# Kernel optimization log

Hardware: AMD Instinct MI355X
Metric: run time of the kernel (lower is better)

Reference implementation:

```python
import jax, jax.numpy as jnp
import numpy as np

N_EMBD = 768
HIDDEN = 4 * N_EMBD
N_EXPERTS = 8
TOP_K = 2


def setup_inputs() -> dict:
    key = jax.random.key(0)
    ks = jax.random.split(key, 4)
    B, T, C, E, H = 4, 2048, N_EMBD, N_EXPERTS, HIDDEN
    x = jax.random.normal(ks[0], (B, T, C), dtype=jnp.float32)
    gate_w = jax.random.normal(ks[1], (E, C), dtype=jnp.float32) * 0.02
    gate_b = jnp.zeros((E,), dtype=jnp.float32)
    w_fc = jax.random.normal(ks[2], (E, H, C), dtype=jnp.float32) * 0.02
    b_fc = jnp.zeros((E, H), dtype=jnp.float32)
    w_proj = jax.random.normal(ks[3], (E, C, H), dtype=jnp.float32) * 0.02
    b_proj = jnp.zeros((E, C), dtype=jnp.float32)
    return {"x": x, "gate_w": gate_w, "gate_b": gate_b, "w_fc": w_fc,
            "b_fc": b_fc, "w_proj": w_proj, "b_proj": b_proj}


def reference(x, gate_w, gate_b, w_fc, b_fc, w_proj, b_proj):
    B, T, C = x.shape
    E = gate_b.shape[0]
    xf = x.reshape(-1, C)  # [N, C]
    # gating: Linear(C -> E), top-k, softmax over the k selected scores
    scores = xf @ gate_w.T + gate_b                      # [N, E]
    top_s, top_i = jax.lax.top_k(scores, TOP_K)          # [N, K]
    gates = jax.nn.softmax(top_s, axis=-1)               # [N, K]
    # combine weight per (token, expert): sum_k gate[t,k] * 1[top_i[t,k]==e]
    comb = jnp.sum(jax.nn.one_hot(top_i, E, dtype=xf.dtype) * gates[..., None], axis=1)  # [N, E]
    out = jnp.zeros_like(xf)
    for j in range(E):  # loop over fixed small expert count
        h = jax.nn.gelu(xf @ w_fc[j].T + b_fc[j], approximate=True)  # [N, H]
        y = h @ w_proj[j].T + b_proj[j]                              # [N, C]
        out = out + comb[:, j:j + 1] * y
    return out.reshape(B, T, C)
```

## Files before the change

### kernel.cpp

```cpp
#include <hip/hip_runtime.h>
#include <cmath>

#define N_TOK 8192
#define C_DIM 768
#define H_DIM 3072
#define NEXP  8
#define PADCAP 17408
#define MAXMT  136

typedef short short8 __attribute__((ext_vector_type(8)));
typedef float f32x4  __attribute__((ext_vector_type(4)));

__device__ __forceinline__ unsigned short f2b(float f) {
  unsigned int u = __float_as_uint(f);
  u += 0x7fffu + ((u >> 16) & 1u);
  return (unsigned short)(u >> 16);
}
__device__ __forceinline__ float b2f(unsigned short u) {
  return __uint_as_float((unsigned int)u << 16);
}
__device__ __forceinline__ void gll(const char* g, char* l) {
  __builtin_amdgcn_global_load_lds((const __attribute__((address_space(1))) void*)g,
                                   (__attribute__((address_space(3))) void*)l, 16, 0, 0);
}

__global__ __launch_bounds__(256) void gate_kernel(
    const float* __restrict__ x, const float* __restrict__ gw,
    const float* __restrict__ gb, int* __restrict__ counts,
    int* __restrict__ tok_e, int* __restrict__ tok_r, float* __restrict__ tok_w) {
  __shared__ float gwl[NEXP * C_DIM];
  __shared__ double red[256][NEXP];
  int tid = threadIdx.x;
  const float4* gw4 = (const float4*)gw;
  float4* gl4 = (float4*)gwl;
  for (int i = tid; i < NEXP * C_DIM / 4; i += 256) gl4[i] = gw4[i];
  __syncthreads();
  int tl = tid & 63;
  int kc = tid >> 6;
  int t = blockIdx.x * 64 + tl;
  double acc[NEXP];
#pragma unroll
  for (int e = 0; e < NEXP; e++) acc[e] = 0.0;
  const float* xr = x + (size_t)t * C_DIM;
  for (int k = kc * 192; k < kc * 192 + 192; k++) {
    double xv = (double)xr[k];
#pragma unroll
    for (int e = 0; e < NEXP; e++) acc[e] += xv * (double)gwl[e * C_DIM + k];
  }
#pragma unroll
  for (int e = 0; e < NEXP; e++) red[tid][e] = acc[e];
  __syncthreads();
  if (tid < 64) {
    double s[NEXP];
#pragma unroll
    for (int e = 0; e < NEXP; e++)
      s[e] = (double)gb[e] + red[tid][e] + red[tid + 64][e] + red[tid + 128][e] + red[tid + 192][e];
    double best = s[0], sec = -1e300; int bi = 0, si = -1;
#pragma unroll
    for (int e = 1; e < NEXP; e++) {
      if (s[e] > best)      { sec = best; si = bi; best = s[e]; bi = e; }
      else if (s[e] > sec)  { sec = s[e]; si = e; }
    }
    double ex = exp(sec - best);
    double den = 1.0 + ex;
    tok_e[2 * t] = bi;  tok_e[2 * t + 1] = si;
    tok_w[2 * t] = (float)(1.0 / den);  tok_w[2 * t + 1] = (float)(ex / den);
    tok_r[2 * t]     = atomicAdd(&counts[bi], 1);
    tok_r[2 * t + 1] = atomicAdd(&counts[si], 1);
  }
}

__global__ void offsets_kernel(const int* __restrict__ counts, int* __restrict__ po) {
  if (threadIdx.x == 0 && blockIdx.x == 0) {
    int s = 0;
    for (int e = 0; e < NEXP; e++) { po[e] = s; s += (counts[e] + 127) & ~127; }
    po[NEXP] = s;
  }
}

__global__ __launch_bounds__(256) void scatter_kernel(
    const int* __restrict__ tok_e, const int* __restrict__ tok_r,
    const float* __restrict__ tok_w, const int* __restrict__ po,
    int* __restrict__ perm_t, float* __restrict__ perm_w,
    int* __restrict__ tok_pos) {
  int t = blockIdx.x * 256 + threadIdx.x;
#pragma unroll
  for (int k = 0; k < 2; k++) {
    int e = tok_e[2 * t + k];
    int pos = po[e] + tok_r[2 * t + k];
    perm_t[pos] = t;
    perm_w[pos] = tok_w[2 * t + k];
    tok_pos[2 * t + k] = pos;
  }
}

__global__ __launch_bounds__(256) void gather_kernel(
    const float* __restrict__ x, const int* __restrict__ po,
    const int* __restrict__ perm_t, unsigned short* __restrict__ xg) {
  int row = blockIdx.x * 4 + (threadIdx.x >> 6);
  if (row >= po[NEXP]) return;
  int l = threadIdx.x & 63;
  int t = perm_t[row];
  const float4* src = (const float4*)(x + (size_t)t * C_DIM);
  ushort4* dst = (ushort4*)(xg + (size_t)row * C_DIM);
#pragma unroll
  for (int j = 0; j < 3; j++) {
    float4 v = src[l + j * 64];
    ushort4 o; o.x = f2b(v.x); o.y = f2b(v.y); o.z = f2b(v.z); o.w = f2b(v.w);
    dst[l + j * 64] = o;
  }
}

__global__ __launch_bounds__(256) void wconv_kernel(
    const float* __restrict__ wfc, const float* __restrict__ wproj,
    unsigned short* __restrict__ wfcb, unsigned short* __restrict__ wpjb) {
  const int n4 = NEXP * H_DIM * C_DIM / 4;
  int stride = gridDim.x * blockDim.x;
  for (int i = blockIdx.x * blockDim.x + threadIdx.x; i < 2 * n4; i += stride) {
    const float4* s; ushort4* d; int j;
    if (i < n4) { s = (const float4*)wfc;   d = (ushort4*)wfcb; j = i; }
    else        { s = (const float4*)wproj; d = (ushort4*)wpjb; j = i - n4; }
    float4 v = s[j];
    ushort4 o; o.x = f2b(v.x); o.y = f2b(v.y); o.z = f2b(v.z); o.w = f2b(v.w);
    d[j] = o;
  }
}

#define STAGE6(kt, bufbase) do {                                   \
    size_t kb_ = (size_t)(kt) * 128;                               \
    char* nb_ = lds + (bufbase);                                   \
    gll(gA0 + kb_, nb_ + wb);                                      \
    gll(gA1 + kb_, nb_ + 8192 + wb);                               \
    gll(gB0p + kb_, nb_ + 16384 + wb);                             \
    gll(gB1p + kb_, nb_ + 24576 + wb);                             \
    gll(gB2p + kb_, nb_ + 32768 + wb);                             \
    gll(gB3p + kb_, nb_ + 40960 + wb);                             \
  } while (0)

__device__ __forceinline__ void gemm_big(
    const unsigned short* A, int lda, const unsigned short* B, int ldb, int K,
    char* lds, int tid, f32x4 acc[4][4]) {
  const int w = tid >> 6, l = tid & 63;
  const int wr = w >> 2, wc = w & 3;
  const int ra0 = wr * 64 + (l & 15);
  const int rb0 = wc * 64 + (l & 15);
  const int kc = l >> 4;
  const int sa0 = (kc ^ ((ra0 >> 1) & 7)) * 16;
  const int sb0 = (kc ^ ((rb0 >> 1) & 7)) * 16;
  const int rA0 = tid >> 3,           cA0 = (tid & 7) ^ ((rA0 >> 1) & 7);
  const int rA1 = (512 + tid) >> 3,   cA1 = ((512 + tid) & 7) ^ ((rA1 >> 1) & 7);
  const int rB0 = tid >> 3,           cB0 = (tid & 7) ^ ((rB0 >> 1) & 7);
  const int rB1 = (512 + tid) >> 3,   cB1 = ((512 + tid) & 7) ^ ((rB1 >> 1) & 7);
  const int rB2 = (1024 + tid) >> 3,  cB2 = ((1024 + tid) & 7) ^ ((rB2 >> 1) & 7);
  const int rB3 = (1536 + tid) >> 3,  cB3 = ((1536 + tid) & 7) ^ ((rB3 >> 1) & 7);
  const char* gA0  = (const char*)(A + (size_t)rA0 * lda) + cA0 * 16;
  const char* gA1  = (const char*)(A + (size_t)rA1 * lda) + cA1 * 16;
  const char* gB0p = (const char*)(B + (size_t)rB0 * ldb) + cB0 * 16;
  const char* gB1p = (const char*)(B + (size_t)rB1 * ldb) + cB1 * 16;
  const char* gB2p = (const char*)(B + (size_t)rB2 * ldb) + cB2 * 16;
  const char* gB3p = (const char*)(B + (size_t)rB3 * ldb) + cB3 * 16;
  const int wb = w * 1024;
  const int iters = K >> 6;
  STAGE6(0, 0);
  STAGE6(1, 49152);
  int bc = 0, bn2 = 98304;
#pragma unroll 1
  for (int kt = 0; kt < iters; kt++) {
    if (kt < iters - 1) asm volatile("s_waitcnt vmcnt(6)\n\ts_barrier" ::: "memory");
    else                asm volatile("s_waitcnt vmcnt(0)\n\ts_barrier" ::: "memory");
    if (kt + 2 < iters) STAGE6(kt + 2, bn2);
    char* bb = lds + bc;
#pragma unroll
    for (int s = 0; s < 2; s++) {
      const int sxa = sa0 ^ (s << 6);
      const int sxb = sb0 ^ (s << 6);
      short8 af[4], bf[4];
#pragma unroll
      for (int mi = 0; mi < 4; mi++)
        af[mi] = *(const short8*)(bb + (ra0 + mi * 16) * 128 + sxa);
#pragma unroll
      for (int ni = 0; ni < 4; ni++)
        bf[ni] = *(const short8*)(bb + 16384 + (rb0 + ni * 16) * 128 + sxb);
      __builtin_amdgcn_s_setprio(1);
#pragma unroll
      for (int mi = 0; mi < 4; mi++)
#pragma unroll
        for (int ni = 0; ni < 4; ni++)
          acc[mi][ni] = __builtin_amdgcn_mfma_f32_16x16x32_bf16(af[mi], bf[ni], acc[mi][ni], 0, 0, 0);
      __builtin_amdgcn_s_setprio(0);
      if (s == 0) asm volatile("s_barrier" ::: "memory");
    }
    bc += 49152;  if (bc == 147456)  bc = 0;
    bn2 += 49152; if (bn2 == 147456) bn2 = 0;
  }
}

__global__ __launch_bounds__(512, 2) void fc1_kernel(
    const unsigned short* __restrict__ xg, const unsigned short* __restrict__ wfcb,
    const float* __restrict__ bfc, const int* __restrict__ po,
    unsigned short* __restrict__ h) {
  __shared__ char lds[147456];
  int bid = blockIdx.x;
  int r8 = bid & 7, g8 = bid >> 3;
  int col = g8 % 12;
  int Sp  = g8 / 12;
  int y   = r8 * 17 + Sp;
  int row0 = y * 128;
  if (row0 >= po[NEXP]) return;
  int e = 0;
#pragma unroll
  for (int i = 1; i < NEXP; i++) if (row0 >= po[i]) e = i;
  int n0 = col * 256;
  int tid = threadIdx.x;
  f32x4 acc[4][4];
#pragma unroll
  for (int mi = 0; mi < 4; mi++)
#pragma unroll
    for (int ni = 0; ni < 4; ni++) acc[mi][ni] = (f32x4){0.f, 0.f, 0.f, 0.f};
  gemm_big(xg + (size_t)row0 * C_DIM, C_DIM,
           wfcb + (size_t)e * H_DIM * C_DIM + (size_t)n0 * C_DIM, C_DIM, C_DIM,
           lds, tid, acc);
  int w = tid >> 6, l = tid & 63;
  int wr = w >> 2, wc = w & 3, q = l >> 4;
  const float* bias = bfc + (size_t)e * H_DIM;
#pragma unroll
  for (int ni = 0; ni < 4; ni++) {
    int colw = n0 + wc * 64 + ni * 16 + (l & 15);
    float bv = bias[colw];
#pragma unroll
    for (int mi = 0; mi < 4; mi++) {
#pragma unroll
      for (int r = 0; r < 4; r++) {
        int row = row0 + wr * 64 + mi * 16 + q * 4 + r;
        float v = acc[mi][ni][r] + bv;
        float z = v * fmaf(0.0356774081f, v * v, 0.7978845608f);
        float ex = __builtin_amdgcn_exp2f(-2.8853900818f * z);
        float g = v * __builtin_amdgcn_rcpf(1.0f + ex);
        h[(size_t)row * H_DIM + colw] = f2b(g);
      }
    }
  }
}

__global__ __launch_bounds__(512, 2) void fc2_kernel(
    const unsigned short* __restrict__ h, const unsigned short* __restrict__ wpjb,
    const float* __restrict__ bproj, const int* __restrict__ po,
    const float* __restrict__ perm_w, unsigned short* __restrict__ part) {
  __shared__ char lds[147456];
  int bid = blockIdx.x;
  int r8 = bid & 7, g8 = bid >> 3;
  int col = g8 % 3;
  int qq  = g8 / 3;
  int z   = qq & 1;
  int Sp  = qq >> 1;
  int y   = r8 * 17 + Sp;
  int row0 = y * 128;
  if (row0 >= po[NEXP]) return;
  int e = 0;
#pragma unroll
  for (int i = 1; i < NEXP; i++) if (row0 >= po[i]) e = i;
  int n0 = col * 256;
  int koff = z * (H_DIM / 2);
  int tid = threadIdx.x;
  f32x4 acc[4][4];
#pragma unroll
  for (int mi = 0; mi < 4; mi++)
#pragma unroll
    for (int ni = 0; ni < 4; ni++) acc[mi][ni] = (f32x4){0.f, 0.f, 0.f, 0.f};
  gemm_big(h + (size_t)row0 * H_DIM + koff, H_DIM,
           wpjb + (size_t)e * C_DIM * H_DIM + (size_t)n0 * H_DIM + koff, H_DIM, H_DIM / 2,
           lds, tid, acc);
  int w = tid >> 6, l = tid & 63;
  int wr = w >> 2, wc = w & 3, q = l >> 4;
  const float* bias = bproj + (size_t)e * C_DIM;
  unsigned short* pz = part + (size_t)z * PADCAP * C_DIM;
#pragma unroll
  for (int mi = 0; mi < 4; mi++) {
#pragma unroll
    for (int r = 0; r < 4; r++) {
      int pos = row0 + wr * 64 + mi * 16 + q * 4 + r;
      float wgt = perm_w[pos];
#pragma unroll
      for (int ni = 0; ni < 4; ni++) {
        int colw = n0 + wc * 64 + ni * 16 + (l & 15);
        float v = acc[mi][ni][r];
        if (z == 0) v += bias[colw];
        pz[(size_t)pos * C_DIM + colw] = f2b(v * wgt);
      }
    }
  }
}

__global__ __launch_bounds__(256) void combine_kernel(
    const unsigned short* __restrict__ part, const int* __restrict__ tok_pos,
    float* __restrict__ out) {
  const int NC4 = C_DIM / 4;
  int idx = blockIdx.x * 256 + threadIdx.x;
  int t = idx / NC4, c4 = idx - t * NC4;
  int p0 = tok_pos[2 * t], p1 = tok_pos[2 * t + 1];
  const size_t SP = (size_t)PADCAP * C_DIM;
  const unsigned short* r00 = part + (size_t)p0 * C_DIM + c4 * 4;
  const unsigned short* r10 = part + (size_t)p1 * C_DIM + c4 * 4;
  ushort4 v00 = *(const ushort4*)r00;
  ushort4 v01 = *(const ushort4*)(r00 + SP);
  ushort4 v10 = *(const ushort4*)r10;
  ushort4 v11 = *(const ushort4*)(r10 + SP);
  float4 o;
  o.x = b2f(v00.x) + b2f(v01.x) + b2f(v10.x) + b2f(v11.x);
  o.y = b2f(v00.y) + b2f(v01.y) + b2f(v10.y) + b2f(v11.y);
  o.z = b2f(v00.z) + b2f(v01.z) + b2f(v10.z) + b2f(v11.z);
  o.w = b2f(v00.w) + b2f(v01.w) + b2f(v10.w) + b2f(v11.w);
  ((float4*)out)[idx] = o;
}

extern "C" void kernel_launch(void* const* d_in, const int* in_sizes, int n_in,
                              void* d_out, int out_size, void* d_ws, size_t ws_size,
                              hipStream_t stream) {
  const float* x     = (const float*)d_in[0];
  const float* gw    = (const float*)d_in[1];
  const float* gb    = (const float*)d_in[2];
  const float* wfc   = (const float*)d_in[3];
  const float* bfc   = (const float*)d_in[4];
  const float* wproj = (const float*)d_in[5];
  const float* bproj = (const float*)d_in[6];
  float* out = (float*)d_out;
  char* ws = (char*)d_ws;

  int*   counts  = (int*)(ws + 0);
  int*   po      = (int*)(ws + 64);
  int*   tok_e   = (int*)(ws + 256);
  int*   tok_r   = (int*)(ws + 65792);
  float* tok_w   = (float*)(ws + 131328);
  int*   tok_pos = (int*)(ws + 196864);
  int*   perm_t  = (int*)(ws + 262400);
  float* perm_w  = (float*)(ws + 332032);
  const size_t ROUT_END = 401920;
  unsigned short* wpjb = (unsigned short*)(ws + 401920);
  unsigned short* hbuf = (unsigned short*)(ws + 38150656);
  unsigned short* xg   = (unsigned short*)(ws + 145105408);
  unsigned short* wfcb = (unsigned short*)(ws + 171844096);
  unsigned short* part = (unsigned short*)(ws + 145105408);

  hipMemsetAsync(ws, 0, ROUT_END, stream);

  gate_kernel<<<N_TOK / 64, 256, 0, stream>>>(x, gw, gb, counts, tok_e, tok_r, tok_w);
  offsets_kernel<<<1, 64, 0, stream>>>(counts, po);
  scatter_kernel<<<N_TOK / 256, 256, 0, stream>>>(tok_e, tok_r, tok_w, po, perm_t, perm_w, tok_pos);
  gather_kernel<<<PADCAP / 4, 256, 0, stream>>>(x, po, perm_t, xg);
  wconv_kernel<<<2048, 256, 0, stream>>>(wfc, wproj, wfcb, wpjb);
  fc1_kernel<<<8 * 17 * 12, 512, 0, stream>>>(xg, wfcb, bfc, po, hbuf);
  fc2_kernel<<<8 * 17 * 3 * 2, 512, 0, stream>>>(hbuf, wpjb, bproj, po, perm_w, part);
  combine_kernel<<<N_TOK * (C_DIM / 4) / 256, 256, 0, stream>>>(part, tok_pos, out);
}
```

Baseline: 533.7 us.

## Switch expert GEMMs to 256x256 tiles with ping-pong LDS schedule

Replaces the 128x256 triple-buffered GEMM core with a 256x256 tile per block, using two 64KB LDS buffers and interleaved quarter-tile MFMA phases that overlap global_load_lds with compute. Expert row padding grows to 256, fc2 drops its K-split so combine reads two partials instead of four, and the weight conversion is split so fc_proj conversion reuses the same workspace after fc1. Larger tiles raise operand reuse and remove the split-K traffic, at the cost of more padding waste, fewer blocks, higher register pressure and less parallelism in fc2.

```diff
diff --git a/kernel.cpp b/kernel.cpp
--- a/kernel.cpp
+++ b/kernel.cpp
@@ -5,8 +5,7 @@
 #define C_DIM 768
 #define H_DIM 3072
 #define NEXP  8
-#define PADCAP 17408
-#define MAXMT  136
+#define PADCAP 18432
 
 typedef short short8 __attribute__((ext_vector_type(8)));
 typedef float f32x4  __attribute__((ext_vector_type(4)));
@@ -73,7 +72,7 @@
 __global__ void offsets_kernel(const int* __restrict__ counts, int* __restrict__ po) {
   if (threadIdx.x == 0 && blockIdx.x == 0) {
     int s = 0;
-    for (int e = 0; e < NEXP; e++) { po[e] = s; s += (counts[e] + 127) & ~127; }
+    for (int e = 0; e < NEXP; e++) { po[e] = s; s += (counts[e] + 255) & ~255; }
     po[NEXP] = s;
   }
 }
@@ -112,126 +111,146 @@
 }
 
 __global__ __launch_bounds__(256) void wconv_kernel(
-    const float* __restrict__ wfc, const float* __restrict__ wproj,
-    unsigned short* __restrict__ wfcb, unsigned short* __restrict__ wpjb) {
-  const int n4 = NEXP * H_DIM * C_DIM / 4;
+    const float* __restrict__ src, unsigned short* __restrict__ dst, int n4) {
   int stride = gridDim.x * blockDim.x;
-  for (int i = blockIdx.x * blockDim.x + threadIdx.x; i < 2 * n4; i += stride) {
-    const float4* s; ushort4* d; int j;
-    if (i < n4) { s = (const float4*)wfc;   d = (ushort4*)wfcb; j = i; }
-    else        { s = (const float4*)wproj; d = (ushort4*)wpjb; j = i - n4; }
-    float4 v = s[j];
+  for (int i = blockIdx.x * blockDim.x + threadIdx.x; i < n4; i += stride) {
+    float4 v = ((const float4*)src)[i];
     ushort4 o; o.x = f2b(v.x); o.y = f2b(v.y); o.z = f2b(v.z); o.w = f2b(v.w);
-    d[j] = o;
-  }
-}
-
-#define STAGE6(kt, bufbase) do {                                   \
-    size_t kb_ = (size_t)(kt) * 128;                               \
-    char* nb_ = lds + (bufbase);                                   \
-    gll(gA0 + kb_, nb_ + wb);                                      \
-    gll(gA1 + kb_, nb_ + 8192 + wb);                               \
-    gll(gB0p + kb_, nb_ + 16384 + wb);                             \
-    gll(gB1p + kb_, nb_ + 24576 + wb);                             \
-    gll(gB2p + kb_, nb_ + 32768 + wb);                             \
-    gll(gB3p + kb_, nb_ + 40960 + wb);                             \
-  } while (0)
-
-__device__ __forceinline__ void gemm_big(
-    const unsigned short* A, int lda, const unsigned short* B, int ldb, int K,
-    char* lds, int tid, f32x4 acc[4][4]) {
+    ((ushort4*)dst)[i] = o;
+  }
+}
+
+__device__ __forceinline__ void gemm8p(
+    const char* __restrict__ Ab, size_t ldaB,
+    const char* __restrict__ Bb, size_t ldbB, int ktiles,
+    char* lds, int tid, f32x4 acc[8][4]) {
   const int w = tid >> 6, l = tid & 63;
   const int wr = w >> 2, wc = w & 3;
-  const int ra0 = wr * 64 + (l & 15);
-  const int rb0 = wc * 64 + (l & 15);
-  const int kc = l >> 4;
-  const int sa0 = (kc ^ ((ra0 >> 1) & 7)) * 16;
-  const int sb0 = (kc ^ ((rb0 >> 1) & 7)) * 16;
-  const int rA0 = tid >> 3,           cA0 = (tid & 7) ^ ((rA0 >> 1) & 7);
-  const int rA1 = (512 + tid) >> 3,   cA1 = ((512 + tid) & 7) ^ ((rA1 >> 1) & 7);
-  const int rB0 = tid >> 3,           cB0 = (tid & 7) ^ ((rB0 >> 1) & 7);
-  const int rB1 = (512 + tid) >> 3,   cB1 = ((512 + tid) & 7) ^ ((rB1 >> 1) & 7);
-  const int rB2 = (1024 + tid) >> 3,  cB2 = ((1024 + tid) & 7) ^ ((rB2 >> 1) & 7);
-  const int rB3 = (1536 + tid) >> 3,  cB3 = ((1536 + tid) & 7) ^ ((rB3 >> 1) & 7);
-  const char* gA0  = (const char*)(A + (size_t)rA0 * lda) + cA0 * 16;
-  const char* gA1  = (const char*)(A + (size_t)rA1 * lda) + cA1 * 16;
-  const char* gB0p = (const char*)(B + (size_t)rB0 * ldb) + cB0 * 16;
-  const char* gB1p = (const char*)(B + (size_t)rB1 * ldb) + cB1 * 16;
-  const char* gB2p = (const char*)(B + (size_t)rB2 * ldb) + cB2 * 16;
-  const char* gB3p = (const char*)(B + (size_t)rB3 * ldb) + cB3 * 16;
-  const int wb = w * 1024;
-  const int iters = K >> 6;
-  STAGE6(0, 0);
-  STAGE6(1, 49152);
-  int bc = 0, bn2 = 98304;
+  const int lr = l & 15, kc = l >> 4;
+  const int sw = (lr >> 1) & 7;
+  const int s0 = ((kc ^ sw) << 4);
+  const int s1 = s0 ^ 64;
+  const int arow = ((wr << 7) + lr) << 7;
+  const int brow = 32768 + (((wc << 6) + lr) << 7);
+  const int rl0 = tid >> 3;
+  const int cg0 = (tid & 7) ^ ((rl0 >> 1) & 7);
+  const size_t oA0 = (size_t)rl0 * ldaB + (cg0 << 4);
+  const size_t oA1 = oA0 + (ldaB << 6);
+  const size_t oB0 = (size_t)rl0 * ldbB + (cg0 << 4);
+  const size_t oB1 = oB0 + (ldbB << 6);
+  const int wb = w << 10;
+
+#define SA(b, h, kt) do { \
+    const char* s_ = Ab + (size_t)(h) * 128 * ldaB + (size_t)(kt) * 128; \
+    gll(s_ + oA0, lds + (b) * 65536 + (h) * 16384 + wb); \
+    gll(s_ + oA1, lds + (b) * 65536 + (h) * 16384 + 8192 + wb); } while (0)
+#define SB(b, h, kt) do { \
+    const char* s_ = Bb + (size_t)(h) * 128 * ldbB + (size_t)(kt) * 128; \
+    gll(s_ + oB0, lds + (b) * 65536 + 32768 + (h) * 16384 + wb); \
+    gll(s_ + oB1, lds + (b) * 65536 + 32768 + (h) * 16384 + 8192 + wb); } while (0)
+#define BAR() asm volatile("s_barrier" ::: "memory")
+#define RDA(B, mb) do { \
+    for (int mi = 0; mi < 4; mi++) { \
+      af[mi][0] = *(const short8*)(lds + (B) + arow + ((mb) + mi) * 2048 + s0); \
+      af[mi][1] = *(const short8*)(lds + (B) + arow + ((mb) + mi) * 2048 + s1); } } while (0)
+#define RDB(B, nb) do { \
+    for (int ni = 0; ni < 2; ni++) { \
+      bf[(nb) + ni][0] = *(const short8*)(lds + (B) + brow + ((nb) + ni) * 2048 + s0); \
+      bf[(nb) + ni][1] = *(const short8*)(lds + (B) + brow + ((nb) + ni) * 2048 + s1); } } while (0)
+#define MM(mb, nb) do { \
+    __builtin_amdgcn_s_setprio(1); \
+    for (int mi = 0; mi < 4; mi++) \
+      for (int ni = 0; ni < 2; ni++) \
+        for (int kk = 0; kk < 2; kk++) \
+          acc[(mb) + mi][(nb) + ni] = __builtin_amdgcn_mfma_f32_16x16x32_bf16( \
+              af[mi][kk], bf[(nb) + ni][kk], acc[(mb) + mi][(nb) + ni], 0, 0, 0); \
+    __builtin_amdgcn_s_setprio(0); } while (0)
+
+  short8 af[4][2], bf[4][2];
+  SB(0, 0, 0); SB(0, 1, 0); SA(0, 0, 0); SA(0, 1, 0);
+  SB(1, 0, 1); SB(1, 1, 1);
+  asm volatile("s_waitcnt vmcnt(4)" ::: "memory");
+  BAR();
+  const int iters = ktiles >> 1;
 #pragma unroll 1
-  for (int kt = 0; kt < iters; kt++) {
-    if (kt < iters - 1) asm volatile("s_waitcnt vmcnt(6)\n\ts_barrier" ::: "memory");
-    else                asm volatile("s_waitcnt vmcnt(0)\n\ts_barrier" ::: "memory");
-    if (kt + 2 < iters) STAGE6(kt + 2, bn2);
-    char* bb = lds + bc;
-#pragma unroll
-    for (int s = 0; s < 2; s++) {
-      const int sxa = sa0 ^ (s << 6);
-      const int sxb = sb0 ^ (s << 6);
-      short8 af[4], bf[4];
-#pragma unroll
-      for (int mi = 0; mi < 4; mi++)
-        af[mi] = *(const short8*)(bb + (ra0 + mi * 16) * 128 + sxa);
-#pragma unroll
-      for (int ni = 0; ni < 4; ni++)
-        bf[ni] = *(const short8*)(bb + 16384 + (rb0 + ni * 16) * 128 + sxb);
-      __builtin_amdgcn_s_setprio(1);
-#pragma unroll
-      for (int mi = 0; mi < 4; mi++)
-#pragma unroll
-        for (int ni = 0; ni < 4; ni++)
-          acc[mi][ni] = __builtin_amdgcn_mfma_f32_16x16x32_bf16(af[mi], bf[ni], acc[mi][ni], 0, 0, 0);
-      __builtin_amdgcn_s_setprio(0);
-      if (s == 0) asm volatile("s_barrier" ::: "memory");
+  for (int i = 0; i < iters; i++) {
+    const int t1 = 2 * i + 1, t2 = 2 * i + 2, t3 = 2 * i + 3;
+    const bool nl = (i + 1 < iters);
+    RDA(0, 0); RDB(0, 0);
+    SA(1, 0, t1);
+    BAR(); MM(0, 0); BAR();
+    RDB(0, 2);
+    SA(1, 1, t1);
+    BAR(); MM(0, 2); BAR();
+    RDA(0, 4);
+    if (nl) SB(0, 0, t2);
+    BAR(); MM(4, 2); BAR();
+    if (nl) SB(0, 1, t2);
+    BAR(); MM(4, 0);
+    if (nl) asm volatile("s_waitcnt vmcnt(4)" ::: "memory");
+    else    asm volatile("s_waitcnt vmcnt(0)" ::: "memory");
+    BAR();
+    RDA(65536, 0); RDB(65536, 0);
+    if (nl) SA(0, 0, t2);
+    BAR(); MM(0, 0); BAR();
+    RDB(65536, 2);
+    if (nl) SA(0, 1, t2);
+    BAR(); MM(0, 2); BAR();
+    RDA(65536, 4);
+    if (nl) SB(1, 0, t3);
+    BAR(); MM(4, 2); BAR();
+    if (nl) SB(1, 1, t3);
+    BAR(); MM(4, 0);
+    if (nl) {
+      asm volatile("s_waitcnt vmcnt(4)" ::: "memory");
+      BAR();
     }
-    bc += 49152;  if (bc == 147456)  bc = 0;
-    bn2 += 49152; if (bn2 == 147456) bn2 = 0;
-  }
+  }
+#undef SA
+#undef SB
+#undef BAR
+#undef RDA
+#undef RDB
+#undef MM
 }
 
 __global__ __launch_bounds__(512, 2) void fc1_kernel(
     const unsigned short* __restrict__ xg, const unsigned short* __restrict__ wfcb,
     const float* __restrict__ bfc, const int* __restrict__ po,
     unsigned short* __restrict__ h) {
-  __shared__ char lds[147456];
+  __shared__ char lds[131072];
   int bid = blockIdx.x;
   int r8 = bid & 7, g8 = bid >> 3;
   int col = g8 % 12;
   int Sp  = g8 / 12;
-  int y   = r8 * 17 + Sp;
-  int row0 = y * 128;
+  int y   = r8 * 9 + Sp;
+  int row0 = y * 256;
   if (row0 >= po[NEXP]) return;
   int e = 0;
 #pragma unroll
   for (int i = 1; i < NEXP; i++) if (row0 >= po[i]) e = i;
   int n0 = col * 256;
   int tid = threadIdx.x;
-  f32x4 acc[4][4];
-#pragma unroll
-  for (int mi = 0; mi < 4; mi++)
+  f32x4 acc[8][4];
+#pragma unroll
+  for (int mi = 0; mi < 8; mi++)
 #pragma unroll
     for (int ni = 0; ni < 4; ni++) acc[mi][ni] = (f32x4){0.f, 0.f, 0.f, 0.f};
-  gemm_big(xg + (size_t)row0 * C_DIM, C_DIM,
-           wfcb + (size_t)e * H_DIM * C_DIM + (size_t)n0 * C_DIM, C_DIM, C_DIM,
-           lds, tid, acc);
+  gemm8p((const char*)(xg + (size_t)row0 * C_DIM), (size_t)C_DIM * 2,
+         (const char*)(wfcb + (size_t)e * H_DIM * C_DIM + (size_t)n0 * C_DIM),
+         (size_t)C_DIM * 2, C_DIM / 64, lds, tid, acc);
   int w = tid >> 6, l = tid & 63;
-  int wr = w >> 2, wc = w & 3, q = l >> 4;
+  int wr = w >> 2, wc = w & 3, lr = l & 15, q = l >> 4;
   const float* bias = bfc + (size_t)e * H_DIM;
 #pragma unroll
   for (int ni = 0; ni < 4; ni++) {
-    int colw = n0 + wc * 64 + ni * 16 + (l & 15);
+    int colw = n0 + wc * 64 + ni * 16 + lr;
     float bv = bias[colw];
 #pragma unroll
-    for (int mi = 0; mi < 4; mi++) {
+    for (int mi = 0; mi < 8; mi++) {
 #pragma unroll
       for (int r = 0; r < 4; r++) {
-        int row = row0 + wr * 64 + mi * 16 + q * 4 + r;
+        int row = row0 + wr * 128 + mi * 16 + q * 4 + r;
         float v = acc[mi][ni][r] + bv;
         float z = v * fmaf(0.0356774081f, v * v, 0.7978845608f);
         float ex = __builtin_amdgcn_exp2f(-2.8853900818f * z);
@@ -246,46 +265,41 @@
     const unsigned short* __restrict__ h, const unsigned short* __restrict__ wpjb,
     const float* __restrict__ bproj, const int* __restrict__ po,
     const float* __restrict__ perm_w, unsigned short* __restrict__ part) {
-  __shared__ char lds[147456];
+  __shared__ char lds[131072];
   int bid = blockIdx.x;
   int r8 = bid & 7, g8 = bid >> 3;
   int col = g8 % 3;
-  int qq  = g8 / 3;
-  int z   = qq & 1;
-  int Sp  = qq >> 1;
-  int y   = r8 * 17 + Sp;
-  int row0 = y * 128;
+  int Sp  = g8 / 3;
+  int y   = r8 * 9 + Sp;
+  int row0 = y * 256;
   if (row0 >= po[NEXP]) return;
   int e = 0;
 #pragma unroll
   for (int i = 1; i < NEXP; i++) if (row0 >= po[i]) e = i;
   int n0 = col * 256;
-  int koff = z * (H_DIM / 2);
   int tid = threadIdx.x;
-  f32x4 acc[4][4];
-#pragma unroll
-  for (int mi = 0; mi < 4; mi++)
+  f32x4 acc[8][4];
+#pragma unroll
+  for (int mi = 0; mi < 8; mi++)
 #pragma unroll
     for (int ni = 0; ni < 4; ni++) acc[mi][ni] = (f32x4){0.f, 0.f, 0.f, 0.f};
-  gemm_big(h + (size_t)row0 * H_DIM + koff, H_DIM,
-           wpjb + (size_t)e * C_DIM * H_DIM + (size_t)n0 * H_DIM + koff, H_DIM, H_DIM / 2,
-           lds, tid, acc);
+  gemm8p((const char*)(h + (size_t)row0 * H_DIM), (size_t)H_DIM * 2,
+         (const char*)(wpjb + (size_t)e * C_DIM * H_DIM + (size_t)n0 * H_DIM),
+         (size_t)H_DIM * 2, H_DIM / 64, lds, tid, acc);
   int w = tid >> 6, l = tid & 63;
-  int wr = w >> 2, wc = w & 3, q = l >> 4;
+  int wr = w >> 2, wc = w & 3, lr = l & 15, q = l >> 4;
   const float* bias = bproj + (size_t)e * C_DIM;
-  unsigned short* pz = part + (size_t)z * PADCAP * C_DIM;
-#pragma unroll
-  for (int mi = 0; mi < 4; mi++) {
+#pragma unroll
+  for (int mi = 0; mi < 8; mi++) {
 #pragma unroll
     for (int r = 0; r < 4; r++) {
-      int pos = row0 + wr * 64 + mi * 16 + q * 4 + r;
+      int pos = row0 + wr * 128 + mi * 16 + q * 4 + r;
       float wgt = perm_w[pos];
 #pragma unroll
       for (int ni = 0; ni < 4; ni++) {
-        int colw = n0 + wc * 64 + ni * 16 + (l & 15);
-        float v = acc[mi][ni][r];
-        if (z == 0) v += bias[colw];
-        pz[(size_t)pos * C_DIM + colw] = f2b(v * wgt);
+        int colw = n0 + wc * 64 + ni * 16 + lr;
+        float v = acc[mi][ni][r] + bias[colw];
+        part[(size_t)pos * C_DIM + colw] = f2b(v * wgt);
       }
     }
   }
@@ -298,18 +312,13 @@
   int idx = blockIdx.x * 256 + threadIdx.x;
   int t = idx / NC4, c4 = idx - t * NC4;
   int p0 = tok_pos[2 * t], p1 = tok_pos[2 * t + 1];
-  const size_t SP = (size_t)PADCAP * C_DIM;
-  const unsigned short* r00 = part + (size_t)p0 * C_DIM + c4 * 4;
-  const unsigned short* r10 = part + (size_t)p1 * C_DIM + c4 * 4;
-  ushort4 v00 = *(const ushort4*)r00;
-  ushort4 v01 = *(const ushort4*)(r00 + SP);
-  ushort4 v10 = *(const ushort4*)r10;
-  ushort4 v11 = *(const ushort4*)(r10 + SP);
+  ushort4 v0 = *(const ushort4*)(part + (size_t)p0 * C_DIM + c4 * 4);
+  ushort4 v1 = *(const ushort4*)(part + (size_t)p1 * C_DIM + c4 * 4);
   float4 o;
-  o.x = b2f(v00.x) + b2f(v01.x) + b2f(v10.x) + b2f(v11.x);
-  o.y = b2f(v00.y) + b2f(v01.y) + b2f(v10.y) + b2f(v11.y);
-  o.z = b2f(v00.z) + b2f(v01.z) + b2f(v10.z) + b2f(v11.z);
-  o.w = b2f(v00.w) + b2f(v01.w) + b2f(v10.w) + b2f(v11.w);
+  o.x = b2f(v0.x) + b2f(v1.x);
+  o.y = b2f(v0.y) + b2f(v1.y);
+  o.z = b2f(v0.z) + b2f(v1.z);
+  o.w = b2f(v0.w) + b2f(v1.w);
   ((float4*)out)[idx] = o;
 }
 
@@ -333,22 +342,24 @@
   float* tok_w   = (float*)(ws + 131328);
   int*   tok_pos = (int*)(ws + 196864);
   int*   perm_t  = (int*)(ws + 262400);
-  float* perm_w  = (float*)(ws + 332032);
-  const size_t ROUT_END = 401920;
-  unsigned short* wpjb = (unsigned short*)(ws + 401920);
-  unsigned short* hbuf = (unsigned short*)(ws + 38150656);
-  unsigned short* xg   = (unsigned short*)(ws + 145105408);
-  unsigned short* wfcb = (unsigned short*)(ws + 171844096);
-  unsigned short* part = (unsigned short*)(ws + 145105408);
+  float* perm_w  = (float*)(ws + 336128);
+  const size_t ROUT_END = 409856;
+  unsigned short* wfcb = (unsigned short*)(ws + 409856);
+  unsigned short* wpjb = (unsigned short*)(ws + 409856);
+  unsigned short* xg   = (unsigned short*)(ws + 38158592);
+  unsigned short* part = (unsigned short*)(ws + 38158592);
+  unsigned short* hbuf = (unsigned short*)(ws + 66470144);
 
   hipMemsetAsync(ws, 0, ROUT_END, stream);
 
+  const int WN4 = NEXP * H_DIM * C_DIM / 4;
   gate_kernel<<<N_TOK / 64, 256, 0, stream>>>(x, gw, gb, counts, tok_e, tok_r, tok_w);
   offsets_kernel<<<1, 64, 0, stream>>>(counts, po);
   scatter_kernel<<<N_TOK / 256, 256, 0, stream>>>(tok_e, tok_r, tok_w, po, perm_t, perm_w, tok_pos);
   gather_kernel<<<PADCAP / 4, 256, 0, stream>>>(x, po, perm_t, xg);
-  wconv_kernel<<<2048, 256, 0, stream>>>(wfc, wproj, wfcb, wpjb);
-  fc1_kernel<<<8 * 17 * 12, 512, 0, stream>>>(xg, wfcb, bfc, po, hbuf);
-  fc2_kernel<<<8 * 17 * 3 * 2, 512, 0, stream>>>(hbuf, wpjb, bproj, po, perm_w, part);
+  wconv_kernel<<<2048, 256, 0, stream>>>(wfc, wfcb, WN4);
+  fc1_kernel<<<8 * 9 * 12, 512, 0, stream>>>(xg, wfcb, bfc, po, hbuf);
+  wconv_kernel<<<2048, 256, 0, stream>>>(wproj, wpjb, WN4);
+  fc2_kernel<<<8 * 9 * 3, 512, 0, stream>>>(hbuf, wpjb, bproj, po, perm_w, part);
   combine_kernel<<<N_TOK * (C_DIM / 4) / 256, 256, 0, stream>>>(part, tok_pos, out);
 }
```

New measurement: 505.7 us. -5.2%, faster.
